# Optimization experiments

Hardware: AMD Instinct MI355X
Metric: run time of the kernel (lower is better)

Reference implementation:

```python
import jax, jax.numpy as jnp
import numpy as np

N = 8192
IN_DIM = 512
MEM_DIM = 512


def _linear_params(k, fan_in, fan_out):
    kw, kb = jax.random.split(k)
    s = 1.0 / np.sqrt(fan_in)
    W = jax.random.uniform(kw, (fan_in, fan_out), jnp.float32, -s, s)
    b = jax.random.uniform(kb, (fan_out,), jnp.float32, -s, s)
    return W, b


def setup_inputs() -> dict:
    key = jax.random.key(0)
    ks = jax.random.split(key, 12)
    inputs = jax.random.normal(ks[0], (N, IN_DIM), jnp.float32)
    # tree.type is a [1,2] mixing matrix per node (lang vs vis weights)
    type_mask = jax.nn.softmax(jax.random.normal(ks[1], (N, 2), jnp.float32), axis=-1)
    # topologically ordered tree: parent slot of node i is in [0, i]; slot 0 = virtual zero root state
    rng = np.random.default_rng(0)
    parent = np.zeros(N, dtype=np.int32)
    for i in range(1, N):
        parent[i] = rng.integers(0, i + 1)
    d = {"inputs": inputs, "type_mask": type_mask, "parent": jnp.asarray(parent)}
    names = ["ioux_vis", "iouh_vis", "fx_vis", "fh_vis",
             "ioux_lang", "iouh_lang", "fx_lang", "fh_lang"]
    fanins = [IN_DIM, MEM_DIM, IN_DIM, MEM_DIM] * 2
    fanouts = [3 * MEM_DIM, 3 * MEM_DIM, MEM_DIM, MEM_DIM] * 2
    for j, nm in enumerate(names):
        W, b = _linear_params(ks[2 + j], fanins[j], fanouts[j])
        d["W_" + nm] = W
        d["b_" + nm] = b
    return d


def reference(inputs, type_mask, parent,
              W_ioux_vis, b_ioux_vis, W_iouh_vis, b_iouh_vis,
              W_fx_vis, b_fx_vis, W_fh_vis, b_fh_vis,
              W_ioux_lang, b_ioux_lang, W_iouh_lang, b_iouh_lang,
              W_fx_lang, b_fx_lang, W_fh_lang, b_fh_lang):
    n_nodes = inputs.shape[0]
    D = W_fh_vis.shape[1]
    # batch the input-dependent projections into big GEMMs (fused across all nodes)
    x_iou_v = inputs @ W_ioux_vis + b_ioux_vis  # [N, 3D]
    x_f_v = inputs @ W_fx_vis + b_fx_vis        # [N, D]
    x_iou_l = inputs @ W_ioux_lang + b_ioux_lang
    x_f_l = inputs @ W_fx_lang + b_fx_lang

    def node(x_iou, x_f, h_p, c_p, W_iouh, b_iouh, W_fh, b_fh):
        iou = x_iou + h_p @ W_iouh + b_iouh  # [3D]
        i, o, u = jnp.split(iou, 3)
        f = jax.nn.sigmoid(x_f + h_p @ W_fh + b_fh)
        c = jax.nn.sigmoid(i) * jnp.tanh(u) + f * c_p
        h = jax.nn.sigmoid(o) * jnp.tanh(c)
        return c, h

    # slot 0 holds the zero state used by root nodes; node i lives at slot i+1
    c0 = jnp.zeros((n_nodes + 1, D), inputs.dtype)
    h0 = jnp.zeros((n_nodes + 1, D), inputs.dtype)

    def step(carry, xs):
        c_all, h_all = carry
        n, p, xiv, xfv, xil, xfl, tm = xs
        h_p = h_all[p]
        c_p = c_all[p]
        c_v, h_v = node(xiv, xfv, h_p, c_p, W_iouh_vis, b_iouh_vis, W_fh_vis, b_fh_vis)
        c_l, h_l = node(xil, xfl, h_p, c_p, W_iouh_lang, b_iouh_lang, W_fh_lang, b_fh_lang)
        # type_mask @ cat([lang, vis]) == tm[0]*lang + tm[1]*vis
        c_n = tm[0] * c_l + tm[1] * c_v
        h_n = tm[0] * h_l + tm[1] * h_v  # dropout is identity in eval
        return (c_all.at[n + 1].set(c_n), h_all.at[n + 1].set(h_n)), None

    idx = jnp.arange(n_nodes)
    (c_all, h_all), _ = jax.lax.scan(
        step, (c0, h0), (idx, parent, x_iou_v, x_f_v, x_iou_l, x_f_l, type_mask))
    return c_all[1:], h_all[1:]
```

## Files before the change

kernel.cpp:

```cpp
#include <hip/hip_runtime.h>
#include <math.h>

typedef unsigned short ushort_t;
typedef unsigned int uint_t;
typedef unsigned long long u64_t;
typedef __attribute__((ext_vector_type(8))) short short8;
typedef __attribute__((ext_vector_type(4))) float f32x4;

#define N_NODES 8192
#define DIM 512
#define KTOT 1024
#define NCOLS 4096
#define BM 128
#define BN 128
#define NTILE (NCOLS / BN)
#define KIT (KTOT / 32)
#define WIMG_USHORTS ((size_t)NTILE * KIT * 4096)
#define MAXLEV_LDS 128

__device__ __forceinline__ float sigm(float x) { return 1.0f / (1.0f + __expf(-x)); }
__device__ __forceinline__ float tanh_fast(float x) {
    float ax = fabsf(x);
    float e = __expf(2.0f * ax);
    float t = 1.0f - 2.0f / (e + 1.0f);
    return copysignf(t, x);
}
__device__ __forceinline__ uint_t packf(float f) {
    uint_t u = __float_as_uint(f);
    uint_t hi = u & 0xffff0000u;
    float r = f - __uint_as_float(hi);
    return hi | (__float_as_uint(r) >> 16);
}
__device__ __forceinline__ uint_t rne16(float f) {
    uint_t u = __float_as_uint(f);
    return (u + 0x7fffu + ((u >> 16) & 1u)) >> 16;
}

__device__ __forceinline__ void fragAB_u32(const uint4 w0, const uint4 w1,
                                           short8& hi8, short8& lo8) {
    union { uint_t w[4]; short8 s; } H, L;
    uint_t u[8] = { w0.x, w0.y, w0.z, w0.w, w1.x, w1.y, w1.z, w1.w };
#pragma unroll
    for (int j = 0; j < 4; ++j) {
        H.w[j] = (u[2 * j + 1] & 0xffff0000u) | (u[2 * j] >> 16);
        L.w[j] = (u[2 * j + 1] << 16) | (u[2 * j] & 0xffffu);
    }
    hi8 = H.s; lo8 = L.s;
}

__device__ __forceinline__ void fragA_f32(const float4 f0, const float4 f1,
                                          short8& hi8, short8& lo8) {
    union { uint_t w[4]; short8 s; } H, L;
    float f[8] = { f0.x, f0.y, f0.z, f0.w, f1.x, f1.y, f1.z, f1.w };
#pragma unroll
    for (int j = 0; j < 4; ++j) {
        float a = f[2 * j], b = f[2 * j + 1];
        uint_t h0 = __float_as_uint(a) & 0xffff0000u;
        uint_t h1 = __float_as_uint(b) & 0xffff0000u;
        float r0 = a - __uint_as_float(h0);
        float r1 = b - __uint_as_float(h1);
        H.w[j] = h1 | (h0 >> 16);
        L.w[j] = (__float_as_uint(r1) & 0xffff0000u) | (__float_as_uint(r0) >> 16);
    }
    hi8 = H.s; lo8 = L.s;
}

__global__ void __launch_bounds__(256) prep_wimg_kernel(
    const float* __restrict__ Wx_iou_v, const float* __restrict__ Wh_iou_v,
    const float* __restrict__ Wx_f_v,   const float* __restrict__ Wh_f_v,
    const float* __restrict__ Wx_iou_l, const float* __restrict__ Wh_iou_l,
    const float* __restrict__ Wx_f_l,   const float* __restrict__ Wh_f_l,
    ushort_t* __restrict__ Wimg)
{
    __shared__ float T[32][132];
    int p = blockIdx.x >> 5, it = blockIdx.x & 31;
    int tid = threadIdx.x;
#pragma unroll
    for (int e = 0; e < 16; ++e) {
        int lin = e * 256 + tid;
        int dloc = lin & 15, kk = (lin >> 4) & 31, q = lin >> 9;
        int d = p * 16 + dloc;
        int qq = q & 3; bool lang = q >= 4;
        int k = it * 32 + kk;
        const float* W; int col, stride;
        if (qq < 3) { col = qq * DIM + d; stride = 3 * DIM;
            W = (k < DIM) ? (lang ? Wx_iou_l : Wx_iou_v) : (lang ? Wh_iou_l : Wh_iou_v); }
        else        { col = d; stride = DIM;
            W = (k < DIM) ? (lang ? Wx_f_l : Wx_f_v) : (lang ? Wh_f_l : Wh_f_v); }
        int kr = (k < DIM) ? k : (k - DIM);
        T[kk][dloc * 8 + q] = W[(size_t)kr * stride + col];
    }
    __syncthreads();
    size_t tilebase = (size_t)blockIdx.x * 4096;
#pragma unroll
    for (int gch = 0; gch < 2; ++gch) {
        int gi = gch * 256 + tid;
        int col = gi >> 2, gd = gi & 3;
        uint_t wds[4];
#pragma unroll
        for (int i = 0; i < 4; ++i) {
            uint_t v0 = rne16(T[gd * 8 + 2 * i][col]);
            uint_t v1 = rne16(T[gd * 8 + 2 * i + 1][col]);
            wds[i] = (v1 << 16) | v0;
        }
        *(uint4*)(Wimg + tilebase + (size_t)gi * 8) = make_uint4(wds[0], wds[1], wds[2], wds[3]);
    }
}

__global__ void prep_bias_kernel(
    const float* __restrict__ bx_iou_v, const float* __restrict__ bh_iou_v,
    const float* __restrict__ bx_f_v,   const float* __restrict__ bh_f_v,
    const float* __restrict__ bx_iou_l, const float* __restrict__ bh_iou_l,
    const float* __restrict__ bx_f_l,   const float* __restrict__ bh_f_l,
    float* __restrict__ bias)
{
    int j = blockIdx.x * blockDim.x + threadIdx.x;
    if (j >= NCOLS) return;
    int d = j >> 3, q = j & 7;
    int qq = q & 3;
    bool lang = (q & 4) != 0;
    const float* bx; const float* bh; int col;
    if (qq < 3) { col = qq * DIM + d; bx = lang ? bx_iou_l : bx_iou_v; bh = lang ? bh_iou_l : bh_iou_v; }
    else        { col = d;            bx = lang ? bx_f_l  : bx_f_v;   bh = lang ? bh_f_l  : bh_f_v; }
    bias[j] = bx[col] + bh[col];
}

__global__ void __launch_bounds__(1024) levels_sort_kernel(
    const int* __restrict__ parent,
    int* __restrict__ order, int* __restrict__ offsets,
    int* __restrict__ counts, int* __restrict__ cursors,
    int* __restrict__ nlev, int* __restrict__ tilestart,
    int* __restrict__ rbStart, int* __restrict__ nodeHrb)
{
    __shared__ int s_level[N_NODES];
    __shared__ int s_assigned;
    __shared__ int s_maxlev;
    int tid = threadIdx.x;
    int pr[8];
#pragma unroll
    for (int ii = 0; ii < 8; ++ii) {
        int i = tid + ii * 1024;
        pr[ii] = parent[i];
        s_level[i] = -1;
    }
    for (int i = tid; i <= N_NODES; i += 1024) counts[i] = 0;
    if (tid == 0) { s_assigned = 0; s_maxlev = 0; }
    __syncthreads();

    for (int pass = 0; pass <= N_NODES; ++pass) {
        int newly = 0;
#pragma unroll
        for (int ii = 0; ii < 8; ++ii) {
            int i = tid + ii * 1024;
            if (s_level[i] < 0) {
                int p = pr[ii];
                if (p == 0) { s_level[i] = 0; newly++; }
                else { int lp = s_level[p - 1]; if (lp >= 0) { s_level[i] = lp + 1; newly++; } }
            }
        }
        if (newly) atomicAdd(&s_assigned, newly);
        __syncthreads();
        int a = s_assigned;
        if (a >= N_NODES) break;
        __syncthreads();
    }

#pragma unroll
    for (int ii = 0; ii < 8; ++ii) {
        int i = tid + ii * 1024;
        int lv = s_level[i];
        atomicAdd(&counts[lv], 1);
        atomicMax(&s_maxlev, lv);
    }
    __syncthreads();
    if (tid == 0) {
        int nl = s_maxlev + 1;
        nlev[0] = nl;
        int off = 0, toff = 0, rb = 0;
        for (int l = 0; l < nl; ++l) {
            offsets[l] = off; cursors[l] = off;
            tilestart[l] = toff; rbStart[l] = rb;
            int mt = (counts[l] + BM - 1) / BM;
            rb += mt;
            toff += mt * NTILE;
            off += counts[l];
        }
        offsets[nl] = off;
        tilestart[nl] = toff;
        rbStart[nl] = rb;
        nlev[1] = toff;
    }
    __syncthreads();
#pragma unroll
    for (int ii = 0; ii < 8; ++ii) {
        int i = tid + ii * 1024;
        int lv = s_level[i];
        int pos = atomicAdd(&cursors[lv], 1);
        order[pos] = i;
        nodeHrb[i] = rbStart[lv] + ((pos - offsets[lv]) >> 7);
    }
}

__global__ void __launch_bounds__(256, 2) tree_fused_kernel(
    const float* __restrict__ inputs, const float* __restrict__ type_mask,
    const ushort_t* __restrict__ Wimg, const float* __restrict__ bias,
    const int* __restrict__ order, const int* __restrict__ offsets,
    const int* __restrict__ nlev, const int* __restrict__ parent,
    const int* __restrict__ rbStart, const int* __restrict__ nodeHrb,
    int* __restrict__ rbCnt,
    uint_t* __restrict__ hPack, uint_t* __restrict__ cPack,
    float* __restrict__ out)
{
    float* cOut = out;
    float* hOut = out + (size_t)N_NODES * DIM;

    __shared__ float eps[BM * 68];
    __shared__ int s_node[BM];
    __shared__ int s_par[BM];
    __shared__ float s_tm[BM][2];
    __shared__ int s_rbs[MAXLEV_LDS];
    __shared__ int s_off[MAXLEV_LDS];

    int tid = threadIdx.x;
    int lane = tid & 63, w = tid >> 6, wr = w >> 1, wc = w & 1;
    int l15 = lane & 15, g = lane >> 4;
    int nl = nlev[0];
    int total = nlev[1];

    int nload = nl + 1; if (nload > MAXLEV_LDS) nload = MAXLEV_LDS;
    for (int i = tid; i < nload; i += 256) { s_rbs[i] = rbStart[i]; s_off[i] = offsets[i]; }
    __syncthreads();

    const ushort_t* bLane = Wimg + (size_t)(wc * 64 + l15) * 32 + (size_t)g * 8;

#define LDB(RB, tilebase, itt) { \
    _Pragma("unroll") for (int n_ = 0; n_ < 4; ++n_) \
        RB[n_] = *(const uint4*)(bLane + (size_t)(tilebase + (itt)) * 4096 + n_ * 512); }

#define LDA_H(RA, itrel) { \
    _Pragma("unroll") for (int m_ = 0; m_ < 4; ++m_) { \
        const uint4* p_ = (const uint4*)(aBaseH[m_] + (itrel) * 32 + g * 8); \
        RA[m_][0] = p_[0]; RA[m_][1] = p_[1]; } }

#define LDA_X(RA, itt) { \
    _Pragma("unroll") for (int m_ = 0; m_ < 4; ++m_) { \
        const float4* p_ = (const float4*)(aBaseX[m_] + (itt) * 32 + g * 8); \
        RA[m_][0] = p_[0]; RA[m_][1] = p_[1]; } }

#define COMP_H(RA, RB) { \
    short8 bh_[4]; \
    _Pragma("unroll") for (int n_ = 0; n_ < 4; ++n_) { \
        union { uint4 u; short8 s; } c_; c_.u = RB[n_]; bh_[n_] = c_.s; } \
    _Pragma("unroll") for (int m_ = 0; m_ < 4; ++m_) { \
        short8 ah_, al_; fragAB_u32(RA[m_][0], RA[m_][1], ah_, al_); \
        _Pragma("unroll") for (int n_ = 0; n_ < 4; ++n_) { \
            acc[m_][n_] = __builtin_amdgcn_mfma_f32_16x16x32_bf16(ah_, bh_[n_], acc[m_][n_], 0, 0, 0); \
            acc[m_][n_] = __builtin_amdgcn_mfma_f32_16x16x32_bf16(al_, bh_[n_], acc[m_][n_], 0, 0, 0); } } }

#define COMP_X(RA, RB) { \
    short8 bh_[4]; \
    _Pragma("unroll") for (int n_ = 0; n_ < 4; ++n_) { \
        union { uint4 u; short8 s; } c_; c_.u = RB[n_]; bh_[n_] = c_.s; } \
    _Pragma("unroll") for (int m_ = 0; m_ < 4; ++m_) { \
        short8 ah_, al_; fragA_f32(RA[m_][0], RA[m_][1], ah_, al_); \
        _Pragma("unroll") for (int n_ = 0; n_ < 4; ++n_) { \
            acc[m_][n_] = __builtin_amdgcn_mfma_f32_16x16x32_bf16(ah_, bh_[n_], acc[m_][n_], 0, 0, 0); \
            acc[m_][n_] = __builtin_amdgcn_mfma_f32_16x16x32_bf16(al_, bh_[n_], acc[m_][n_], 0, 0, 0); } } }

    for (int t = blockIdx.x; t < total; t += gridDim.x) {
        int lev = 0;
        while (lev + 1 < nload && s_rbs[lev + 1] * NTILE <= t) ++lev;
        int lt = t - s_rbs[lev] * NTILE;
        int ntile = lt % NTILE;
        int mt = lt / NTILE;
        int start = s_off[lev];
        int cnt = s_off[lev + 1] - start;
        int jc = ntile * BN;
        int r0 = mt * BM;
        int myhrb = s_rbs[lev] + mt;
        int tbx = ntile * KIT;
        int tbh = ntile * KIT + 16;

        if (tid < BM) {
            int r = r0 + tid;
            int node = (r < cnt) ? order[start + r] : -1;
            s_node[tid] = node;
            int p = (node >= 0) ? parent[node] : 0;
            s_par[tid] = p;
            float t0 = 0.f, t1 = 0.f;
            if (node >= 0) { t0 = type_mask[node * 2]; t1 = type_mask[node * 2 + 1]; }
            s_tm[tid][0] = t0; s_tm[tid][1] = t1;
        }
        __syncthreads();

        f32x4 acc[4][4];
#pragma unroll
        for (int m = 0; m < 4; ++m)
#pragma unroll
            for (int n = 0; n < 4; ++n) acc[m][n] = (f32x4)(0.f);

        {
            const float* aBaseX[4];
#pragma unroll
            for (int m = 0; m < 4; ++m) {
                int nd = s_node[wr * 64 + m * 16 + l15];
                aBaseX[m] = inputs + (size_t)(nd < 0 ? 0 : nd) * DIM;
            }
            float4 xa0[4][2], xa1[4][2]; uint4 xb0[4], xb1[4];
            LDA_X(xa0, 0); LDB(xb0, tbx, 0);
#pragma unroll
            for (int ii = 0; ii < 8; ++ii) {
                int e = 2 * ii, o = e + 1;
                LDA_X(xa1, o); LDB(xb1, tbx, o);
                __builtin_amdgcn_s_setprio(1);
                COMP_X(xa0, xb0);
                __builtin_amdgcn_s_setprio(0);
                if (e + 2 < 16) { LDA_X(xa0, e + 2); LDB(xb0, tbx, e + 2); }
                __builtin_amdgcn_s_setprio(1);
                COMP_X(xa1, xb1);
                __builtin_amdgcn_s_setprio(0);
            }
        }

        if (lev > 0) {
            uint4 ha0[4][2], ha1[4][2]; uint4 hb0[4], hb1[4];
            LDB(hb0, tbh, 0); LDB(hb1, tbh, 1);

            {
                int rb0 = s_rbs[lev - 1];
                int nPrev = s_rbs[lev] - rb0;
                if (tid < nPrev) {
                    while (__hip_atomic_load(&rbCnt[rb0 + tid], __ATOMIC_RELAXED,
                                             __HIP_MEMORY_SCOPE_AGENT) < NTILE)
                        __builtin_amdgcn_s_sleep(16);
                }
            }
            __syncthreads();

            const uint_t* aBaseH[4];
#pragma unroll
            for (int m = 0; m < 4; ++m) {
                int p = s_par[wr * 64 + m * 16 + l15];
                aBaseH[m] = hPack + (size_t)((p > 0) ? (p - 1) : 0) * DIM;
            }

            LDA_H(ha0, 0); LDA_H(ha1, 1);
#pragma unroll
            for (int ii = 0; ii < 8; ++ii) {
                int e = 2 * ii, o = e + 1;
                __builtin_amdgcn_s_setprio(1);
                COMP_H(ha0, hb0);
                __builtin_amdgcn_s_setprio(0);
                if (e + 2 < 16) { LDA_H(ha0, e + 2); LDB(hb0, tbh, e + 2); }
                __builtin_amdgcn_s_setprio(1);
                COMP_H(ha1, hb1);
                __builtin_amdgcn_s_setprio(0);
                if (o + 2 < 16) { LDA_H(ha1, o + 2); LDB(hb1, tbh, o + 2); }
            }
        }

        int cntloc = cnt - r0; if (cntloc > BM) cntloc = BM;
        __syncthreads();
#pragma unroll
        for (int pass = 0; pass < 2; ++pass) {
            if (wc == pass) {
#pragma unroll
                for (int m = 0; m < 4; ++m)
#pragma unroll
                    for (int n = 0; n < 4; ++n) {
                        int row = wr * 64 + m * 16 + g * 4;
                        int c = n * 16 + l15;
#pragma unroll
                        for (int r = 0; r < 4; ++r) eps[(row + r) * 68 + c] = acc[m][n][r];
                    }
            }
            __syncthreads();
#pragma unroll
            for (int e = 0; e < 4; ++e) {
                int task = e * 256 + tid;
                int row = task >> 3, dl = task & 7;
                if (row < cntloc) {
                    int node = s_node[row]; int p = s_par[row];
                    const float* ep = &eps[row * 68 + dl * 8];
                    float4 v0 = *(const float4*)ep;
                    float4 v1 = *(const float4*)(ep + 4);
                    int jb = jc + pass * 64 + dl * 8;
                    float4 b0 = *(const float4*)(bias + jb);
                    float4 b1 = *(const float4*)(bias + jb + 4);
                    int d = jb >> 3;
                    float cp = 0.f;
                    if (p > 0) {
                        uint_t wrd = cPack[(size_t)(p - 1) * DIM + d];
                        cp = __uint_as_float(wrd & 0xffff0000u) + __uint_as_float(wrd << 16);
                    }
                    float cv = sigm(v0.x + b0.x) * tanh_fast(v0.z + b0.z)
                             + sigm(v0.w + b0.w) * cp;
                    float hv = sigm(v0.y + b0.y) * tanh_fast(cv);
                    float cl = sigm(v1.x + b1.x) * tanh_fast(v1.z + b1.z)
                             + sigm(v1.w + b1.w) * cp;
                    float hl = sigm(v1.y + b1.y) * tanh_fast(cl);
                    float tm0 = s_tm[row][0], tm1 = s_tm[row][1];
                    float cn = tm0 * cl + tm1 * cv;
                    float hn2 = tm0 * hl + tm1 * hv;
                    size_t oi = (size_t)node * DIM + d;
                    __hip_atomic_store(&cPack[oi], packf(cn),
                                       __ATOMIC_RELAXED, __HIP_MEMORY_SCOPE_AGENT);
                    __hip_atomic_store(&hPack[oi], packf(hn2),
                                       __ATOMIC_RELAXED, __HIP_MEMORY_SCOPE_AGENT);
                    cOut[oi] = cn;
                    hOut[oi] = hn2;
                }
            }
            __syncthreads();
        }

        __builtin_amdgcn_s_waitcnt(0);
        __syncthreads();
        if (tid == 0)
            __hip_atomic_fetch_add(&rbCnt[myhrb], 1, __ATOMIC_RELAXED,
                                   __HIP_MEMORY_SCOPE_AGENT);
    }
#undef LDB
#undef LDA_H
#undef LDA_X
#undef COMP_H
#undef COMP_X
}

extern "C" void kernel_launch(void* const* d_in, const int* in_sizes, int n_in,
                              void* d_out, int out_size, void* d_ws, size_t ws_size,
                              hipStream_t stream) {
    const float* inputs      = (const float*)d_in[0];
    const float* type_mask   = (const float*)d_in[1];
    const int*   parent      = (const int*)d_in[2];
    const float* W_ioux_vis  = (const float*)d_in[3];
    const float* b_ioux_vis  = (const float*)d_in[4];
    const float* W_iouh_vis  = (const float*)d_in[5];
    const float* b_iouh_vis  = (const float*)d_in[6];
    const float* W_fx_vis    = (const float*)d_in[7];
    const float* b_fx_vis    = (const float*)d_in[8];
    const float* W_fh_vis    = (const float*)d_in[9];
    const float* b_fh_vis    = (const float*)d_in[10];
    const float* W_ioux_lang = (const float*)d_in[11];
    const float* b_ioux_lang = (const float*)d_in[12];
    const float* W_iouh_lang = (const float*)d_in[13];
    const float* b_iouh_lang = (const float*)d_in[14];
    const float* W_fx_lang   = (const float*)d_in[15];
    const float* b_fx_lang   = (const float*)d_in[16];
    const float* W_fh_lang   = (const float*)d_in[17];
    const float* b_fh_lang   = (const float*)d_in[18];

    ushort_t* Wimg = (ushort_t*)d_ws;
    float* bias    = (float*)(Wimg + WIMG_USHORTS);
    int* order     = (int*)(bias + NCOLS);
    int* offsets   = order + N_NODES;
    int* counts    = offsets + (N_NODES + 2);
    int* cursors   = counts + (N_NODES + 2);
    int* nlev      = cursors + (N_NODES + 2);
    int* tilestart = nlev + 8;
    int* rbStart   = tilestart + (N_NODES + 2);
    int* nodeHrb   = rbStart + (N_NODES + 2);
    int* rbCnt     = nodeHrb + N_NODES;
    size_t off2 = (size_t)((char*)(rbCnt + 4096) - (char*)d_ws);
    off2 = (off2 + 255) & ~(size_t)255;
    uint_t* hPack = (uint_t*)((char*)d_ws + off2);
    uint_t* cPack = hPack + (size_t)N_NODES * DIM;

    float* out = (float*)d_out;

    hipMemsetAsync((void*)rbCnt, 0, 4096 * sizeof(int), stream);

    hipLaunchKernelGGL(prep_wimg_kernel, dim3(NTILE * KIT), dim3(256), 0, stream,
                       W_ioux_vis, W_iouh_vis, W_fx_vis, W_fh_vis,
                       W_ioux_lang, W_iouh_lang, W_fx_lang, W_fh_lang, Wimg);
    hipLaunchKernelGGL(prep_bias_kernel, dim3(NCOLS / 256), dim3(256), 0, stream,
                       b_ioux_vis, b_iouh_vis, b_fx_vis, b_fh_vis,
                       b_ioux_lang, b_iouh_lang, b_fx_lang, b_fh_lang, bias);
    hipLaunchKernelGGL(levels_sort_kernel, dim3(1), dim3(1024), 0, stream,
                       parent, order, offsets, counts, cursors, nlev, tilestart,
                       rbStart, nodeHrb);

    int occ = 0;
    if (hipOccupancyMaxActiveBlocksPerMultiprocessor(&occ, (const void*)tree_fused_kernel, 256, 0) != hipSuccess || occ < 1)
        occ = 1;
    int bpc = occ < 2 ? occ : 2;
    dim3 grid(256 * bpc);

    void* args[] = { (void*)&inputs, (void*)&type_mask, (void*)&Wimg, (void*)&bias,
                     (void*)&order, (void*)&offsets, (void*)&nlev, (void*)&parent,
                     (void*)&rbStart, (void*)&nodeHrb, (void*)&rbCnt,
                     (void*)&hPack, (void*)&cPack, (void*)&out };
    hipLaunchCooperativeKernel((const void*)tree_fused_kernel, grid, dim3(256), args, 0, stream);
}
```

Baseline: 902.5 us.

## Replace per-row-block dependency counters with per-column-tile counters and staged K-group waits

The inter-level dependency wait changes from per-row-block counters (all 32 column tiles of a row block done) to per-column-tile counters for each level. The H-GEMM now waits only for the column groups whose K slice it is about to load, polling again between K steps. This lets consumers start on partial results of the previous level instead of waiting for whole row blocks. The cost is extra block-wide syncs and LDS polling inside the K loop, plus a coarser count per column over all row blocks of the previous level.

Result: faster. 815.1 us (-9.7%).

```diff
diff --git a/kernel.cpp b/kernel.cpp
--- a/kernel.cpp
+++ b/kernel.cpp
@@ -206,8 +206,8 @@
     const ushort_t* __restrict__ Wimg, const float* __restrict__ bias,
     const int* __restrict__ order, const int* __restrict__ offsets,
     const int* __restrict__ nlev, const int* __restrict__ parent,
-    const int* __restrict__ rbStart, const int* __restrict__ nodeHrb,
-    int* __restrict__ rbCnt,
+    const int* __restrict__ rbStart,
+    int* __restrict__ colCnt,
     uint_t* __restrict__ hPack, uint_t* __restrict__ cPack,
     float* __restrict__ out)
 {
@@ -220,6 +220,8 @@
     __shared__ float s_tm[BM][2];
     __shared__ int s_rbs[MAXLEV_LDS];
     __shared__ int s_off[MAXLEV_LDS];
+    __shared__ int s_cok[32];
+    __shared__ int s_ok[8];
 
     int tid = threadIdx.x;
     int lane = tid & 63, w = tid >> 6, wr = w >> 1, wc = w & 1;
@@ -266,6 +268,21 @@
         _Pragma("unroll") for (int n_ = 0; n_ < 4; ++n_) { \
             acc[m_][n_] = __builtin_amdgcn_mfma_f32_16x16x32_bf16(ah_, bh_[n_], acc[m_][n_], 0, 0, 0); \
             acc[m_][n_] = __builtin_amdgcn_mfma_f32_16x16x32_bf16(al_, bh_[n_], acc[m_][n_], 0, 0, 0); } } }
+
+#define WAIT_GROUPS(colPrev, nPrev, gq) { \
+    for (;;) { \
+        if (tid < 32) \
+            s_cok[tid] = (__hip_atomic_load(&(colPrev)[tid], __ATOMIC_RELAXED, \
+                                            __HIP_MEMORY_SCOPE_AGENT) >= (nPrev)) ? 1 : 0; \
+        __syncthreads(); \
+        if (tid < 8) { \
+            if (s_cok[4 * tid] && s_cok[4 * tid + 1] && s_cok[4 * tid + 2] && s_cok[4 * tid + 3]) \
+                s_ok[tid] = 1; \
+        } \
+        __syncthreads(); \
+        if (s_ok[gq]) break; \
+        __builtin_amdgcn_s_sleep(8); \
+    } }
 
     for (int t = blockIdx.x; t < total; t += gridDim.x) {
         int lev = 0;
@@ -277,7 +294,6 @@
         int cnt = s_off[lev + 1] - start;
         int jc = ntile * BN;
         int r0 = mt * BM;
-        int myhrb = s_rbs[lev] + mt;
         int tbx = ntile * KIT;
         int tbh = ntile * KIT + 16;
 
@@ -291,6 +307,8 @@
             if (node >= 0) { t0 = type_mask[node * 2]; t1 = type_mask[node * 2 + 1]; }
             s_tm[tid][0] = t0; s_tm[tid][1] = t1;
         }
+        if (tid < 32) s_cok[tid] = 0;
+        if (tid < 8) s_ok[tid] = 0;
         __syncthreads();
 
         f32x4 acc[4][4];
@@ -323,19 +341,13 @@
         }
 
         if (lev > 0) {
+            const int* colPrev = colCnt + (lev - 1) * NTILE;
+            int nPrev = s_rbs[lev] - s_rbs[lev - 1];
+
             uint4 ha0[4][2], ha1[4][2]; uint4 hb0[4], hb1[4];
             LDB(hb0, tbh, 0); LDB(hb1, tbh, 1);
 
-            {
-                int rb0 = s_rbs[lev - 1];
-                int nPrev = s_rbs[lev] - rb0;
-                if (tid < nPrev) {
-                    while (__hip_atomic_load(&rbCnt[rb0 + tid], __ATOMIC_RELAXED,
-                                             __HIP_MEMORY_SCOPE_AGENT) < NTILE)
-                        __builtin_amdgcn_s_sleep(16);
-                }
-            }
-            __syncthreads();
+            WAIT_GROUPS(colPrev, nPrev, 0);
 
             const uint_t* aBaseH[4];
 #pragma unroll
@@ -343,7 +355,6 @@
                 int p = s_par[wr * 64 + m * 16 + l15];
                 aBaseH[m] = hPack + (size_t)((p > 0) ? (p - 1) : 0) * DIM;
             }
-
             LDA_H(ha0, 0); LDA_H(ha1, 1);
 #pragma unroll
             for (int ii = 0; ii < 8; ++ii) {
@@ -351,11 +362,14 @@
                 __builtin_amdgcn_s_setprio(1);
                 COMP_H(ha0, hb0);
                 __builtin_amdgcn_s_setprio(0);
-                if (e + 2 < 16) { LDA_H(ha0, e + 2); LDB(hb0, tbh, e + 2); }
+                if (ii < 7) {
+                    if (!s_ok[ii + 1]) WAIT_GROUPS(colPrev, nPrev, ii + 1);
+                    LDA_H(ha0, e + 2); LDB(hb0, tbh, e + 2);
+                }
                 __builtin_amdgcn_s_setprio(1);
                 COMP_H(ha1, hb1);
                 __builtin_amdgcn_s_setprio(0);
-                if (o + 2 < 16) { LDA_H(ha1, o + 2); LDB(hb1, tbh, o + 2); }
+                if (ii < 7) { LDA_H(ha1, o + 2); LDB(hb1, tbh, o + 2); }
             }
         }
 
@@ -417,14 +431,15 @@
         __builtin_amdgcn_s_waitcnt(0);
         __syncthreads();
         if (tid == 0)
-            __hip_atomic_fetch_add(&rbCnt[myhrb], 1, __ATOMIC_RELAXED,
-                                   __HIP_MEMORY_SCOPE_AGENT);
+            __hip_atomic_fetch_add(&colCnt[lev * NTILE + ntile], 1,
+                                   __ATOMIC_RELAXED, __HIP_MEMORY_SCOPE_AGENT);
     }
 #undef LDB
 #undef LDA_H
 #undef LDA_X
 #undef COMP_H
 #undef COMP_X
+#undef WAIT_GROUPS
 }
 
 extern "C" void kernel_launch(void* const* d_in, const int* in_sizes, int n_in,
@@ -460,15 +475,15 @@
     int* tilestart = nlev + 8;
     int* rbStart   = tilestart + (N_NODES + 2);
     int* nodeHrb   = rbStart + (N_NODES + 2);
-    int* rbCnt     = nodeHrb + N_NODES;
-    size_t off2 = (size_t)((char*)(rbCnt + 4096) - (char*)d_ws);
+    int* colCnt    = nodeHrb + N_NODES;
+    size_t off2 = (size_t)((char*)(colCnt + MAXLEV_LDS * NTILE) - (char*)d_ws);
     off2 = (off2 + 255) & ~(size_t)255;
     uint_t* hPack = (uint_t*)((char*)d_ws + off2);
     uint_t* cPack = hPack + (size_t)N_NODES * DIM;
 
     float* out = (float*)d_out;
 
-    hipMemsetAsync((void*)rbCnt, 0, 4096 * sizeof(int), stream);
+    hipMemsetAsync((void*)colCnt, 0, MAXLEV_LDS * NTILE * sizeof(int), stream);
 
     hipLaunchKernelGGL(prep_wimg_kernel, dim3(NTILE * KIT), dim3(256), 0, stream,
                        W_ioux_vis, W_iouh_vis, W_fx_vis, W_fh_vis,
@@ -488,7 +503,7 @@
 
     void* args[] = { (void*)&inputs, (void*)&type_mask, (void*)&Wimg, (void*)&bias,
                      (void*)&order, (void*)&offsets, (void*)&nlev, (void*)&parent,
-                     (void*)&rbStart, (void*)&nodeHrb, (void*)&rbCnt,
+                     (void*)&rbStart, (void*)&colCnt,
                      (void*)&hPack, (void*)&cPack, (void*)&out };
     hipLaunchCooperativeKernel((const void*)tree_fused_kernel, grid, dim3(256), args, 0, stream);
 }
```
